# Optimization experiments

Hardware: AMD Instinct MI355X
Metric: run time of the kernel (lower is better)

## Reference

```python
import jax, jax.numpy as jnp
import numpy as np

NUM_HEADS = 32
ROPE_BASE = 10000.0


def _rotate_half(x):
    h = x.shape[-1] // 2
    return jnp.concatenate([-x[..., h:], x[..., :h]], axis=-1)


def setup_inputs() -> dict:
    key = jax.random.key(0)
    ks = jax.random.split(key, 6)
    B, S, H = 2, 2048, 4096
    hidden_states = jax.random.normal(ks[0], (B, S, H), dtype=jnp.float32)
    # additive causal mask: 0 on/below diagonal, large negative above
    causal = jnp.tril(jnp.ones((S, S), dtype=bool))
    attention_mask = jnp.where(causal, 0.0, -1e9).astype(jnp.float32)
    attention_mask = jnp.broadcast_to(attention_mask[None, None], (B, 1, S, S))
    position_ids = jnp.broadcast_to(jnp.arange(S, dtype=jnp.int64 if jax.config.jax_enable_x64 else jnp.int32)[None, :], (B, S))
    scale = 1.0 / np.sqrt(H)
    Wq = jax.random.normal(ks[1], (H, H), dtype=jnp.float32) * scale
    Wk = jax.random.normal(ks[2], (H, H), dtype=jnp.float32) * scale
    Wv = jax.random.normal(ks[3], (H, H), dtype=jnp.float32) * scale
    Wo = jax.random.normal(ks[4], (H, H), dtype=jnp.float32) * scale
    return {"hidden_states": hidden_states, "attention_mask": attention_mask,
            "position_ids": position_ids, "Wq": Wq, "Wk": Wk, "Wv": Wv, "Wo": Wo}


def reference(hidden_states, attention_mask, position_ids, Wq, Wk, Wv, Wo):
    B, S, H = hidden_states.shape
    nh = NUM_HEADS
    hd = H // nh
    # QKV projections (torch Linear: y = x @ W.T), split heads -> [B, nh, S, hd]
    def proj(W):
        y = jnp.einsum('bsh,oh->bso', hidden_states, W)
        return y.reshape(B, S, nh, hd).transpose(0, 2, 1, 3)
    q, k, v = proj(Wq), proj(Wk), proj(Wv)
    # rotary embeddings gathered at position_ids
    inv_freq = 1.0 / (ROPE_BASE ** (jnp.arange(0, hd, 2, dtype=jnp.float32) / hd))
    freqs = position_ids.astype(jnp.float32)[:, :, None] * inv_freq[None, None, :]  # [B,S,hd/2]
    emb = jnp.concatenate([freqs, freqs], axis=-1)  # [B,S,hd]
    cos = jnp.cos(emb)[:, None, :, :]  # [B,1,S,hd]
    sin = jnp.sin(emb)[:, None, :, :]
    q = q * cos + _rotate_half(q) * sin
    k = k * cos + _rotate_half(k) * sin
    # scaled dot-product attention
    scores = jnp.einsum('bhqd,bhkd->bhqk', q, k) / jnp.sqrt(jnp.float32(hd))
    scores = scores + attention_mask
    scores = jnp.maximum(scores, jnp.finfo(scores.dtype).min)
    attn = jax.nn.softmax(scores, axis=-1)
    out = jnp.einsum('bhqk,bhkd->bhqd', attn, v)  # [B,nh,S,hd]
    out = out.transpose(0, 2, 1, 3).reshape(B, S, H)
    return jnp.einsum('bsh,oh->bso', out, Wo)
```

## Files before the change

kernel.cpp:

```cpp
#include <hip/hip_runtime.h>
#include <cstdint>
#include <cmath>

typedef __bf16 bf16;
typedef __bf16 bf16x8 __attribute__((ext_vector_type(8)));
typedef __bf16 bf16x4 __attribute__((ext_vector_type(4)));
typedef float f32x4 __attribute__((ext_vector_type(4)));

#define B_ 2
#define S_ 2048
#define H_ 4096
#define NH 32
#define HD 128

#define VMCNT(n) asm volatile("s_waitcnt vmcnt(" #n ")" ::: "memory")
#define BAR() __builtin_amdgcn_s_barrier()

__device__ __forceinline__ void gl_lds16(const void* g, void* l) {
  __builtin_amdgcn_global_load_lds(
      (const __attribute__((address_space(1))) unsigned int*)g,
      (__attribute__((address_space(3))) unsigned int*)l, 16, 0, 0);
}

__global__ __launch_bounds__(256) void cast_kernel(const float* __restrict__ in,
                                                   bf16* __restrict__ out, int n4) {
  int i = blockIdx.x * 256 + threadIdx.x;
  if (i < n4) {
    float4 v = ((const float4*)in)[i];
    bf16x4 o = {(bf16)v.x, (bf16)v.y, (bf16)v.z, (bf16)v.w};
    ((bf16x4*)out)[i] = o;
  }
}

template <int TM, int TN>
__device__ __forceinline__ void mfma_quad(f32x4 (&acc)[8][4], bf16x8 (&af)[4][2],
                                          bf16x8 (&bfr)[2][2]) {
  __builtin_amdgcn_s_setprio(1);
#pragma unroll
  for (int i = 0; i < 4; ++i)
#pragma unroll
    for (int j = 0; j < 2; ++j)
#pragma unroll
      for (int kf = 0; kf < 2; ++kf)
        acc[TM * 4 + i][TN * 2 + j] = __builtin_amdgcn_mfma_f32_16x16x32_bf16(
            af[i][kf], bfr[j][kf], acc[TM * 4 + i][TN * 2 + j], 0, 0, 0);
  __builtin_amdgcn_s_setprio(0);
}

template <int EPI>
__global__ __launch_bounds__(512, 2) void gemm256(const bf16* __restrict__ A,
                                                  const bf16* __restrict__ Bw,
                                                  void* __restrict__ Cout) {
  constexpr int K = 4096, N = 4096, KT = K / 64;
  __shared__ __attribute__((aligned(16))) char lds[131072];
  char* Al = lds;
  char* Bl = lds + 65536;
  int tid = threadIdx.x;
  int l = tid & 63, lr = l & 15, lg = l >> 4;
  int w = tid >> 6, wm = w >> 2, wn = w & 3;
  int bid = (int)blockIdx.x;
  int swb = (bid & 7) * 32 + (bid >> 3);
  int r0 = (swb >> 4) * 256, c0 = (swb & 15) * 256;
  const bf16* Ab = A + (size_t)r0 * K;
  const bf16* Bb = Bw + (size_t)c0 * K;

  int t16 = (tid * 16) ^ (((tid >> 5) & 1) << 5);
  int lr0 = t16 >> 7;
  int cel = (t16 & 127) >> 1;

  auto stageA = [&](int buf, int mh, int k0) {
    char* dst = Al + buf * 32768 + mh * 16384 + tid * 16;
    int ra = mh * 64 + lr0;
    gl_lds16(Ab + (size_t)ra * K + k0 + cel, dst);
    gl_lds16(Ab + (size_t)(ra + 128) * K + k0 + cel, dst + 8192);
  };
  auto stageB = [&](int buf, int nh, int k0) {
    char* dst = Bl + buf * 32768 + nh * 16384 + tid * 16;
    int n0 = (lr0 >> 5) * 64 + nh * 32 + (lr0 & 31);
    gl_lds16(Bb + (size_t)n0 * K + k0 + cel, dst);
    gl_lds16(Bb + (size_t)(n0 + 128) * K + k0 + cel, dst + 8192);
  };

  bf16x8 af[4][2], bfr[2][2];
  int sw = ((lr >> 2) & 1) << 5;
  auto ldA = [&](int buf, int mh) {
    char* base = Al + buf * 32768 + mh * 16384 + wm * 8192;
#pragma unroll
    for (int mfl = 0; mfl < 4; ++mfl)
#pragma unroll
      for (int kf = 0; kf < 2; ++kf)
        __builtin_memcpy(&af[mfl][kf],
                         base + (mfl * 16 + lr) * 128 + ((kf * 64 + lg * 16) ^ sw), 16);
  };
  auto ldB = [&](int buf, int nh) {
    char* base = Bl + buf * 32768 + nh * 16384 + wn * 4096;
#pragma unroll
    for (int nfl = 0; nfl < 2; ++nfl)
#pragma unroll
      for (int kf = 0; kf < 2; ++kf)
        __builtin_memcpy(&bfr[nfl][kf],
                         base + (nfl * 16 + lr) * 128 + ((kf * 64 + lg * 16) ^ sw), 16);
  };

  f32x4 acc[8][4] = {};

  stageA(0, 0, 0);
  stageB(0, 0, 0);
  stageB(0, 1, 0);
  stageA(0, 1, 0);

  for (int kt = 0; kt < KT - 1; ++kt) {
    int buf = kt & 1, nb = buf ^ 1;
    int k0n = (kt + 1) * 64;
    VMCNT(4); BAR();
    ldA(buf, 0); ldB(buf, 0);
    stageA(nb, 0, k0n);
    mfma_quad<0, 0>(acc, af, bfr);
    BAR();
    VMCNT(4); BAR();
    ldB(buf, 1);
    stageB(nb, 0, k0n);
    mfma_quad<0, 1>(acc, af, bfr);
    BAR();
    VMCNT(4); BAR();
    ldA(buf, 1);
    stageB(nb, 1, k0n);
    mfma_quad<1, 1>(acc, af, bfr);
    BAR();
    BAR();
    ldB(buf, 0);
    stageA(nb, 1, k0n);
    mfma_quad<1, 0>(acc, af, bfr);
    BAR();
  }
  {
    int buf = (KT - 1) & 1;
    VMCNT(4); BAR();
    ldA(buf, 0); ldB(buf, 0);
    mfma_quad<0, 0>(acc, af, bfr);
    BAR();
    VMCNT(2); BAR();
    ldB(buf, 1);
    mfma_quad<0, 1>(acc, af, bfr);
    BAR();
    VMCNT(0); BAR();
    ldA(buf, 1);
    mfma_quad<1, 1>(acc, af, bfr);
    BAR();
    BAR();
    ldB(buf, 0);
    mfma_quad<1, 0>(acc, af, bfr);
  }

#pragma unroll
  for (int mf = 0; mf < 8; ++mf)
#pragma unroll
    for (int nf = 0; nf < 4; ++nf) {
      int orow = r0 + wm * 128 + mf * 16 + lg * 4;
      int ocol = c0 + wn * 64 + nf * 16 + lr;
      if (EPI == 0) {
        bf16* C = (bf16*)Cout;
#pragma unroll
        for (int jr = 0; jr < 4; ++jr)
          C[(size_t)(orow + jr) * N + ocol] = (bf16)acc[mf][nf][jr];
      } else {
        float* C = (float*)Cout;
#pragma unroll
        for (int jr = 0; jr < 4; ++jr)
          C[(size_t)(orow + jr) * N + ocol] = acc[mf][nf][jr];
      }
    }
}

__global__ __launch_bounds__(256) void rope_kernel(bf16* __restrict__ X,
                                                   const int* __restrict__ pos,
                                                   float scale) {
  int r = blockIdx.x;
  float pf = (float)pos[r];
  int i = threadIdx.x & 63;
  int h0 = threadIdx.x >> 6;
  float ang = pf * exp2f(-0.20762050593046868f * (float)i);
  float sn = sinf(ang), cs = cosf(ang);
  bf16* row = X + (size_t)r * H_;
#pragma unroll
  for (int h = h0; h < NH; h += 4) {
    bf16* p = row + h * HD + i;
    float a = (float)p[0], b = (float)p[64];
    p[0] = (bf16)((a * cs - b * sn) * scale);
    p[64] = (bf16)((b * cs + a * sn) * scale);
  }
}

__global__ __launch_bounds__(256) void transpose_v(const bf16* __restrict__ V,
                                                   bf16* __restrict__ Vt) {
  __shared__ __attribute__((aligned(16))) bf16 tile[64][130];
  int bh = blockIdx.y;
  int b = bh >> 5, h = bh & 31;
  int s0 = blockIdx.x * 64;
  int t = threadIdx.x;
  const bf16* src = V + (size_t)(b * S_ + s0) * H_ + h * HD;
  int rr = t >> 4, cc = (t & 15) * 8;
#pragma unroll
  for (int k = 0; k < 4; ++k) {
    bf16x8 v;
    __builtin_memcpy(&v, src + (size_t)(rr + k * 16) * H_ + cc, 16);
#pragma unroll
    for (int u = 0; u < 8; ++u) tile[rr + k * 16][cc + u] = v[u];
  }
  __syncthreads();
  bf16* dst = Vt + (size_t)bh * HD * S_;
  int sl = t & 63, d0 = t >> 6;
  for (int j = 0; j < 32; ++j) {
    int d = d0 + j * 4;
    dst[(size_t)d * S_ + s0 + sl] = tile[sl][d];
  }
}

__global__ __launch_bounds__(512, 4) void attn_kernel(const bf16* __restrict__ Q,
                                                      const bf16* __restrict__ Km,
                                                      const bf16* __restrict__ Vt,
                                                      bf16* __restrict__ Out) {
  __shared__ __attribute__((aligned(16))) bf16 Ks[2][64 * 128];
  __shared__ __attribute__((aligned(16))) bf16 Vs[2][128 * 64];
  __shared__ __attribute__((aligned(16))) bf16 P_lds[8][16 * 64];
  int tid = threadIdx.x;
  int w = tid >> 6, l = tid & 63;
  int lr = l & 15, lg = l >> 4;
  int bh = blockIdx.y, b = bh >> 5, h = bh & 31;
  int qt = 15 - (int)blockIdx.x;
  int q0w = qt * 128 + w * 16;
  const bf16* Qb = Q + (size_t)b * S_ * H_ + h * HD;
  const char* Kg = (const char*)(Km + (size_t)b * S_ * H_ + h * HD);
  const char* Vg = (const char*)(Vt + (size_t)bh * HD * S_);
  bf16* Ob = Out + (size_t)b * S_ * H_ + h * HD;

  bf16x8 qf[4];
#pragma unroll
  for (int dk = 0; dk < 4; ++dk)
    __builtin_memcpy(&qf[dk], Qb + (size_t)(q0w + lr) * H_ + dk * 32 + lg * 8, 16);

  f32x4 o[8] = {};
  float m = -INFINITY, ls = 0.f;
  int nkv_blk = 2 * qt + 2;
  int nkv_w = 2 * qt + (w >> 2) + 1;

  auto stageK = [&](int buf, int kv0) {
#pragma unroll
    for (int p = 0; p < 2; ++p) {
      int row = p * 32 + (tid >> 4);
      int src = ((tid & 15) * 16) ^ ((row & 7) << 4);
      gl_lds16(Kg + (size_t)(kv0 + row) * (H_ * 2) + src,
               (char*)&Ks[buf][0] + p * 8192 + w * 1024);
    }
  };
  auto stageV = [&](int buf, int kv0) {
#pragma unroll
    for (int p = 0; p < 2; ++p) {
      int row = p * 64 + (tid >> 3);
      int src = ((tid & 7) * 16) ^ ((row & 7) << 4);
      gl_lds16(Vg + (size_t)row * (S_ * 2) + (size_t)kv0 * 2 + src,
               (char*)&Vs[buf][0] + p * 8192 + w * 1024);
    }
  };

  stageK(0, 0);
  stageV(0, 0);
  __syncthreads();

  int cur = 0;
  char* Pl = (char*)&P_lds[w][0];
  for (int t = 0; t < nkv_blk; ++t) {
    int kv0 = t * 64;
    if (t + 1 < nkv_blk) {
      stageK(cur ^ 1, kv0 + 64);
      stageV(cur ^ 1, kv0 + 64);
    }
    if (t < nkv_w) {
      const char* Kl = (const char*)&Ks[cur][0];
      const char* Vl = (const char*)&Vs[cur][0];
      f32x4 s4[4] = {};
      __builtin_amdgcn_s_setprio(1);
#pragma unroll
      for (int dk = 0; dk < 4; ++dk)
#pragma unroll
        for (int st = 0; st < 4; ++st) {
          int row = st * 16 + lr;
          int cb = (dk * 64 + lg * 16) ^ ((row & 7) << 4);
          bf16x8 kf;
          __builtin_memcpy(&kf, Kl + row * 256 + cb, 16);
          s4[st] = __builtin_amdgcn_mfma_f32_16x16x32_bf16(kf, qf[dk], s4[st], 0, 0, 0);
        }
      __builtin_amdgcn_s_setprio(0);
      if (t == nkv_w - 1) {
        int qg = q0w + lr;
#pragma unroll
        for (int st = 0; st < 4; ++st)
#pragma unroll
          for (int j = 0; j < 4; ++j)
            if (kv0 + st * 16 + lg * 4 + j > qg) s4[st][j] = -INFINITY;
      }
      float mx = -INFINITY;
#pragma unroll
      for (int st = 0; st < 4; ++st)
#pragma unroll
        for (int j = 0; j < 4; ++j) mx = fmaxf(mx, s4[st][j]);
      mx = fmaxf(mx, __shfl_xor(mx, 16));
      mx = fmaxf(mx, __shfl_xor(mx, 32));
      float sc = 1.0f;
      if (!__all((int)(mx <= m + 8.0f))) {
        float mn = fmaxf(m, mx);
        sc = exp2f(m - mn);
        m = mn;
        float scq0 = __shfl(sc, lg * 4 + 0);
        float scq1 = __shfl(sc, lg * 4 + 1);
        float scq2 = __shfl(sc, lg * 4 + 2);
        float scq3 = __shfl(sc, lg * 4 + 3);
#pragma unroll
        for (int dt = 0; dt < 8; ++dt) {
          o[dt][0] *= scq0; o[dt][1] *= scq1; o[dt][2] *= scq2; o[dt][3] *= scq3;
        }
      }
      float pv[4][4], rs = 0.f;
#pragma unroll
      for (int st = 0; st < 4; ++st)
#pragma unroll
        for (int j = 0; j < 4; ++j) {
          pv[st][j] = exp2f(s4[st][j] - m);
          rs += pv[st][j];
        }
      rs += __shfl_xor(rs, 16);
      rs += __shfl_xor(rs, 32);
      ls = ls * sc + rs;
#pragma unroll
      for (int st = 0; st < 4; ++st) {
        bf16x4 pk = {(bf16)pv[st][0], (bf16)pv[st][1], (bf16)pv[st][2], (bf16)pv[st][3]};
        *(bf16x4*)(Pl + lr * 128 + ((st * 32 + lg * 8) ^ ((lr & 7) << 4))) = pk;
      }
      bf16x8 pa[2];
#pragma unroll
      for (int ks = 0; ks < 2; ++ks)
        __builtin_memcpy(&pa[ks], Pl + lr * 128 + ((ks * 64 + lg * 16) ^ ((lr & 7) << 4)), 16);
      __builtin_amdgcn_s_setprio(1);
#pragma unroll
      for (int dt = 0; dt < 8; ++dt)
#pragma unroll
        for (int ks = 0; ks < 2; ++ks) {
          int row = dt * 16 + lr;
          int cb = (ks * 64 + lg * 16) ^ ((row & 7) << 4);
          bf16x8 vf;
          __builtin_memcpy(&vf, Vl + row * 128 + cb, 16);
          o[dt] = __builtin_amdgcn_mfma_f32_16x16x32_bf16(pa[ks], vf, o[dt], 0, 0, 0);
        }
      __builtin_amdgcn_s_setprio(0);
    }
    __syncthreads();
    cur ^= 1;
  }
  float lsq[4];
#pragma unroll
  for (int j = 0; j < 4; ++j) lsq[j] = __shfl(ls, lg * 4 + j);
#pragma unroll
  for (int j = 0; j < 4; ++j) {
    float inv = 1.0f / lsq[j];
#pragma unroll
    for (int dt = 0; dt < 8; ++dt)
      Ob[(size_t)(q0w + lg * 4 + j) * H_ + dt * 16 + lr] = (bf16)(o[dt][j] * inv);
  }
}

extern "C" void kernel_launch(void* const* d_in, const int* in_sizes, int n_in,
                              void* d_out, int out_size, void* d_ws, size_t ws_size,
                              hipStream_t stream) {
  const float* X = (const float*)d_in[0];
  const int* pos = (const int*)d_in[2];
  const float* Wq = (const float*)d_in[3];
  const float* Wk = (const float*)d_in[4];
  const float* Wv = (const float*)d_in[5];
  const float* Wo = (const float*)d_in[6];
  float* out = (float*)d_out;
  char* ws = (char*)d_ws;
  const size_t MB32 = 32ull << 20;
  bf16* Xb = (bf16*)ws;
  bf16* Wb = (bf16*)(ws + MB32);
  bf16* Qb = (bf16*)(ws + 2 * MB32);
  bf16* Kb = (bf16*)(ws + 3 * MB32);
  bf16* Vb = (bf16*)(ws + 4 * MB32);
  bf16* Vt = (bf16*)(ws + 5 * MB32);

  const int n4 = (4096 * 4096) / 4;
  dim3 cgrid(n4 / 256), cblk(256);
  dim3 ggrid(256), gblk(512);

  cast_kernel<<<cgrid, cblk, 0, stream>>>(X, Xb, n4);
  cast_kernel<<<cgrid, cblk, 0, stream>>>(Wq, Wb, n4);
  gemm256<0><<<ggrid, gblk, 0, stream>>>(Xb, Wb, Qb);
  cast_kernel<<<cgrid, cblk, 0, stream>>>(Wk, Wb, n4);
  gemm256<0><<<ggrid, gblk, 0, stream>>>(Xb, Wb, Kb);
  cast_kernel<<<cgrid, cblk, 0, stream>>>(Wv, Wb, n4);
  gemm256<0><<<ggrid, gblk, 0, stream>>>(Xb, Wb, Vb);

  const float qscale = 1.4426950408889634f / 11.313708498984760f;
  rope_kernel<<<dim3(4096), 256, 0, stream>>>(Qb, pos, qscale);
  rope_kernel<<<dim3(4096), 256, 0, stream>>>(Kb, pos, 1.0f);
  transpose_v<<<dim3(32, 64), 256, 0, stream>>>(Vb, Vt);

  attn_kernel<<<dim3(16, 64), 512, 0, stream>>>(Qb, Kb, Vt, Xb);

  cast_kernel<<<cgrid, cblk, 0, stream>>>(Wo, Wb, n4);
  gemm256<1><<<ggrid, gblk, 0, stream>>>(Xb, Wb, out);
}
```

Before: 921.5 us.

## Double-buffer GEMM register fragments and merge Q/K RoPE launches

The GEMM main loop now keeps two sets of A and B register fragments, so LDS reads for the next sub-tile are issued before the current MFMA group runs. It also prefetches the first fragments of the next K-tile at the end of each iteration, and cuts the barriers per iteration from seven to three. The aim is to hide LDS read latency behind MFMA work and reduce sync stalls, at the cost of more VGPRs, which could spill or hurt occupancy under launch_bounds(512,2). Separately, the two RoPE launches for Q and K are merged into one launch with a 2D grid to save a kernel launch.

```diff
diff --git a/kernel.cpp b/kernel.cpp
--- a/kernel.cpp
+++ b/kernel.cpp
@@ -33,8 +33,8 @@
 }
 
 template <int TM, int TN>
-__device__ __forceinline__ void mfma_quad(f32x4 (&acc)[8][4], bf16x8 (&af)[4][2],
-                                          bf16x8 (&bfr)[2][2]) {
+__device__ __forceinline__ void mfma_q(f32x4 (&acc)[8][4], bf16x8 (&a)[4][2],
+                                       bf16x8 (&b)[2][2]) {
   __builtin_amdgcn_s_setprio(1);
 #pragma unroll
   for (int i = 0; i < 4; ++i)
@@ -43,7 +43,7 @@
 #pragma unroll
       for (int kf = 0; kf < 2; ++kf)
         acc[TM * 4 + i][TN * 2 + j] = __builtin_amdgcn_mfma_f32_16x16x32_bf16(
-            af[i][kf], bfr[j][kf], acc[TM * 4 + i][TN * 2 + j], 0, 0, 0);
+            a[i][kf], b[j][kf], acc[TM * 4 + i][TN * 2 + j], 0, 0, 0);
   __builtin_amdgcn_s_setprio(0);
 }
 
@@ -68,88 +68,79 @@
   int lr0 = t16 >> 7;
   int cel = (t16 & 127) >> 1;
 
-  auto stageA = [&](int buf, int mh, int k0) {
-    char* dst = Al + buf * 32768 + mh * 16384 + tid * 16;
+  auto stageA = [&](int bufB, int mh, int k0) {
+    char* dst = Al + bufB + mh * 16384 + tid * 16;
     int ra = mh * 64 + lr0;
     gl_lds16(Ab + (size_t)ra * K + k0 + cel, dst);
     gl_lds16(Ab + (size_t)(ra + 128) * K + k0 + cel, dst + 8192);
   };
-  auto stageB = [&](int buf, int nh, int k0) {
-    char* dst = Bl + buf * 32768 + nh * 16384 + tid * 16;
+  auto stageB = [&](int bufB, int nh, int k0) {
+    char* dst = Bl + bufB + nh * 16384 + tid * 16;
     int n0 = (lr0 >> 5) * 64 + nh * 32 + (lr0 & 31);
     gl_lds16(Bb + (size_t)n0 * K + k0 + cel, dst);
     gl_lds16(Bb + (size_t)(n0 + 128) * K + k0 + cel, dst + 8192);
   };
 
-  bf16x8 af[4][2], bfr[2][2];
   int sw = ((lr >> 2) & 1) << 5;
-  auto ldA = [&](int buf, int mh) {
-    char* base = Al + buf * 32768 + mh * 16384 + wm * 8192;
+  auto ldA = [&](bf16x8 (&dst)[4][2], int bufB, int mh) {
+    char* base = Al + bufB + mh * 16384 + wm * 8192;
 #pragma unroll
     for (int mfl = 0; mfl < 4; ++mfl)
 #pragma unroll
       for (int kf = 0; kf < 2; ++kf)
-        __builtin_memcpy(&af[mfl][kf],
+        __builtin_memcpy(&dst[mfl][kf],
                          base + (mfl * 16 + lr) * 128 + ((kf * 64 + lg * 16) ^ sw), 16);
   };
-  auto ldB = [&](int buf, int nh) {
-    char* base = Bl + buf * 32768 + nh * 16384 + wn * 4096;
+  auto ldB = [&](bf16x8 (&dst)[2][2], int bufB, int nh) {
+    char* base = Bl + bufB + nh * 16384 + wn * 4096;
 #pragma unroll
     for (int nfl = 0; nfl < 2; ++nfl)
 #pragma unroll
       for (int kf = 0; kf < 2; ++kf)
-        __builtin_memcpy(&bfr[nfl][kf],
+        __builtin_memcpy(&dst[nfl][kf],
                          base + (nfl * 16 + lr) * 128 + ((kf * 64 + lg * 16) ^ sw), 16);
   };
 
+  bf16x8 afA[4][2], afB[4][2], bf0[2][2], bf1[2][2];
   f32x4 acc[8][4] = {};
 
   stageA(0, 0, 0);
   stageB(0, 0, 0);
   stageB(0, 1, 0);
   stageA(0, 1, 0);
+  VMCNT(4); BAR();
+  ldA(afA, 0, 0);
+  ldB(bf0, 0, 0);
 
   for (int kt = 0; kt < KT - 1; ++kt) {
-    int buf = kt & 1, nb = buf ^ 1;
+    int cur = (kt & 1) << 15, nxt = cur ^ 32768;
     int k0n = (kt + 1) * 64;
-    VMCNT(4); BAR();
-    ldA(buf, 0); ldB(buf, 0);
-    stageA(nb, 0, k0n);
-    mfma_quad<0, 0>(acc, af, bfr);
-    BAR();
-    VMCNT(4); BAR();
-    ldB(buf, 1);
-    stageB(nb, 0, k0n);
-    mfma_quad<0, 1>(acc, af, bfr);
-    BAR();
-    VMCNT(4); BAR();
-    ldA(buf, 1);
-    stageB(nb, 1, k0n);
-    mfma_quad<1, 1>(acc, af, bfr);
-    BAR();
-    BAR();
-    ldB(buf, 0);
-    stageA(nb, 1, k0n);
-    mfma_quad<1, 0>(acc, af, bfr);
-    BAR();
+    VMCNT(2); BAR();
+    ldB(bf1, cur, 1);
+    stageA(nxt, 0, k0n);
+    mfma_q<0, 0>(acc, afA, bf0);
+    VMCNT(2); BAR();
+    ldA(afB, cur, 1);
+    stageB(nxt, 0, k0n);
+    mfma_q<0, 1>(acc, afA, bf1);
+    stageB(nxt, 1, k0n);
+    mfma_q<1, 1>(acc, afB, bf1);
+    VMCNT(2); BAR();
+    stageA(nxt, 1, k0n);
+    mfma_q<1, 0>(acc, afB, bf0);
+    ldA(afA, nxt, 0);
+    ldB(bf0, nxt, 0);
   }
   {
-    int buf = (KT - 1) & 1;
-    VMCNT(4); BAR();
-    ldA(buf, 0); ldB(buf, 0);
-    mfma_quad<0, 0>(acc, af, bfr);
-    BAR();
+    int cur = ((KT - 1) & 1) << 15;
     VMCNT(2); BAR();
-    ldB(buf, 1);
-    mfma_quad<0, 1>(acc, af, bfr);
-    BAR();
+    ldB(bf1, cur, 1);
+    mfma_q<0, 0>(acc, afA, bf0);
     VMCNT(0); BAR();
-    ldA(buf, 1);
-    mfma_quad<1, 1>(acc, af, bfr);
-    BAR();
-    BAR();
-    ldB(buf, 0);
-    mfma_quad<1, 0>(acc, af, bfr);
+    ldA(afB, cur, 1);
+    mfma_q<0, 1>(acc, afA, bf1);
+    mfma_q<1, 1>(acc, afB, bf1);
+    mfma_q<1, 0>(acc, afB, bf0);
   }
 
 #pragma unroll
@@ -172,10 +163,13 @@
     }
 }
 
-__global__ __launch_bounds__(256) void rope_kernel(bf16* __restrict__ X,
+__global__ __launch_bounds__(256) void rope_kernel(bf16* __restrict__ Qx,
+                                                   bf16* __restrict__ Kx,
                                                    const int* __restrict__ pos,
-                                                   float scale) {
+                                                   float qscale) {
   int r = blockIdx.x;
+  bf16* X = blockIdx.y ? Kx : Qx;
+  float scale = blockIdx.y ? 1.0f : qscale;
   float pf = (float)pos[r];
   int i = threadIdx.x & 63;
   int h0 = threadIdx.x >> 6;
@@ -400,8 +394,7 @@
   gemm256<0><<<ggrid, gblk, 0, stream>>>(Xb, Wb, Vb);
 
   const float qscale = 1.4426950408889634f / 11.313708498984760f;
-  rope_kernel<<<dim3(4096), 256, 0, stream>>>(Qb, pos, qscale);
-  rope_kernel<<<dim3(4096), 256, 0, stream>>>(Kb, pos, 1.0f);
+  rope_kernel<<<dim3(4096, 2), 256, 0, stream>>>(Qb, Kb, pos, qscale);
   transpose_v<<<dim3(32, 64), 256, 0, stream>>>(Vb, Vt);
 
   attn_kernel<<<dim3(16, 64), 512, 0, stream>>>(Qb, Kb, Vt, Xb);
```

Measured after the change: 3.628 ms. 294% more time.
